# Kernel tuning notes

Measured on AMD Instinct MI355X. Metric: run time of the kernel, lower is better.

## Reference

```python
import jax, jax.numpy as jnp
import numpy as np
import math

D_MODEL = 1024
N_HEADS = 16
D_HEAD = D_MODEL // N_HEADS
D_FF = 4096
BATCH = 2
SEQ = 2048
EPS = 1e-5


def _rmsnorm(x, w):
    rms = jnp.sqrt(jnp.mean(x * x, axis=-1, keepdims=True) + EPS)
    return (x / rms) * w


def _gelu_erf(x):
    # matches 0.5 * x * (1 + erf(x / sqrt(2)))
    return 0.5 * x * (1.0 + jax.lax.erf(x / jnp.sqrt(jnp.asarray(2.0, x.dtype))))


def setup_inputs() -> dict:
    key = jax.random.key(0)
    ks = jax.random.split(key, 6)
    scale = 0.02
    x = jax.random.normal(ks[0], (BATCH, SEQ, D_MODEL), dtype=jnp.float32)
    w_qkv = jax.random.normal(ks[1], (3 * D_MODEL, D_MODEL), dtype=jnp.float32) * scale
    w_o = jax.random.normal(ks[2], (D_MODEL, D_MODEL), dtype=jnp.float32) * scale
    ln1_w = jnp.ones((D_MODEL,), dtype=jnp.float32)
    ln2_w = jnp.ones((D_MODEL,), dtype=jnp.float32)
    w1 = jax.random.normal(ks[3], (D_FF, D_MODEL), dtype=jnp.float32) * scale
    w2 = jax.random.normal(ks[4], (D_MODEL, D_FF), dtype=jnp.float32) * scale
    return {"x": x, "w_qkv": w_qkv, "w_o": w_o, "ln1_w": ln1_w,
            "ln2_w": ln2_w, "w1": w1, "w2": w2}


def reference(x, w_qkv, w_o, ln1_w, ln2_w, w1, w2):
    B, S, D = x.shape
    # --- attention sublayer (pre-norm) ---
    h = _rmsnorm(x, ln1_w)
    qkv = jnp.einsum('bsd,ed->bse', h, w_qkv)            # (B,S,3*D)
    qkv = qkv.reshape(B, S, 3, N_HEADS, D_HEAD)
    q, k, v = jnp.moveaxis(qkv, 2, 0)                    # each (B,S,H,dh)
    q = q.transpose(0, 2, 1, 3)                          # (B,H,S,dh)
    k = k.transpose(0, 2, 1, 3)
    v = v.transpose(0, 2, 1, 3)
    scores = jnp.einsum('bhqd,bhkd->bhqk', q, k) / math.sqrt(D_HEAD)
    causal = jnp.tril(jnp.ones((S, S), dtype=bool))      # True = keep
    scores = jnp.where(causal, scores, jnp.asarray(-jnp.inf, scores.dtype))
    attn = jax.nn.softmax(scores, axis=-1)
    ctx = jnp.einsum('bhqk,bhkd->bhqd', attn, v)         # (B,H,S,dh)
    ctx = ctx.transpose(0, 2, 1, 3).reshape(B, S, D)
    attn_out = jnp.einsum('bsd,ed->bse', ctx, w_o)
    first_sum = x + attn_out
    # --- FFN sublayer (pre-norm) ---
    h2 = _rmsnorm(first_sum, ln2_w)
    ff = jnp.einsum('bsf,df->bsd', _gelu_erf(jnp.einsum('bsd,fd->bsf', h2, w1)), w2)
    return first_sum + ff
```

## Files before the change

kernel.cpp:

```cpp
#include <hip/hip_runtime.h>

typedef unsigned short u16;
typedef unsigned int u32;
typedef __attribute__((ext_vector_type(8))) short short8;
typedef __attribute__((ext_vector_type(4))) float f32x4;

#define AS1 __attribute__((address_space(1)))
#define AS3 __attribute__((address_space(3)))

__device__ __forceinline__ u16 f2bf(float f) {
  union { float f; unsigned u; } v; v.f = f;
  return (u16)((v.u + 0x7fffu + ((v.u >> 16) & 1u)) >> 16);
}
__device__ __forceinline__ u32 pack2bf(float a, float b) {
  return (u32)f2bf(a) | ((u32)f2bf(b) << 16);
}
__device__ __forceinline__ u32 permpack(float a, float b) {
  union { float f; u32 u; } ua, ub; ua.f = a; ub.f = b;
  return __builtin_amdgcn_perm(ub.u, ua.u, 0x07060302u);
}

__global__ void cvt_kernel(const float* __restrict__ in, u16* __restrict__ out,
                           float scale) {
  int i = (blockIdx.x * 256 + threadIdx.x) * 4;
  float4 v = *(const float4*)(in + i);
  ushort4 o = make_ushort4(f2bf(v.x * scale), f2bf(v.y * scale),
                           f2bf(v.z * scale), f2bf(v.w * scale));
  *(ushort4*)(out + i) = o;
}

__global__ void rmsnorm_kernel(const float* __restrict__ x, const float* __restrict__ w,
                               u16* __restrict__ out) {
  const int row = blockIdx.x, tid = threadIdx.x;
  const float4 v = ((const float4*)(x + (size_t)row * 1024))[tid];
  float ss = v.x * v.x + v.y * v.y + v.z * v.z + v.w * v.w;
#pragma unroll
  for (int off = 32; off > 0; off >>= 1) ss += __shfl_xor(ss, off);
  __shared__ float red[4];
  if ((tid & 63) == 0) red[tid >> 6] = ss;
  __syncthreads();
  float tot = red[0] + red[1] + red[2] + red[3];
  float scale = 1.0f / sqrtf(tot * (1.0f / 1024.0f) + 1e-5f);
  const float4 wv = ((const float4*)w)[tid];
  ushort4 o = make_ushort4(f2bf(v.x * scale * wv.x), f2bf(v.y * scale * wv.y),
                           f2bf(v.z * scale * wv.z), f2bf(v.w * scale * wv.w));
  ((ushort4*)(out + (size_t)row * 1024))[tid] = o;
}

template <int EPI>
__global__ __launch_bounds__(256)
void gemm_bt(const u16* __restrict__ A, const u16* __restrict__ B,
             const float* __restrict__ RES, void* __restrict__ OUT,
             int M, int N, int K) {
  __shared__ __align__(16) u16 As[128 * 32];
  __shared__ __align__(16) u16 Bs[128 * 32];
  const int tid = threadIdx.x;
  const int wave = tid >> 6, lane = tid & 63;
  const int quad = lane >> 4, l16 = lane & 15;
  const int m0 = blockIdx.y * 128, n0 = blockIdx.x * 128;
  const int wm = (wave >> 1) * 64, wn = (wave & 1) * 64;
  f32x4 acc[4][4] = {};

  const int c0 = wave * 128 + lane;
  const int r0_row = c0 >> 2, r0_col = (c0 & 3) * 8;
  const int c1 = c0 + 64;
  const int r1_row = c1 >> 2, r1_col = (c1 & 3) * 8;

  for (int k0 = 0; k0 < K; k0 += 32) {
    __syncthreads();
    {
      u16* ga0 = (u16*)(A + (size_t)(m0 + r0_row) * K + k0 + r0_col);
      u16* ga1 = (u16*)(A + (size_t)(m0 + r1_row) * K + k0 + r1_col);
      u16* gb0 = (u16*)(B + (size_t)(n0 + r0_row) * K + k0 + r0_col);
      u16* gb1 = (u16*)(B + (size_t)(n0 + r1_row) * K + k0 + r1_col);
      __builtin_amdgcn_global_load_lds((AS1 void*)ga0, (AS3 void*)(As + wave * 1024), 16, 0, 0);
      __builtin_amdgcn_global_load_lds((AS1 void*)ga1, (AS3 void*)(As + wave * 1024 + 512), 16, 0, 0);
      __builtin_amdgcn_global_load_lds((AS1 void*)gb0, (AS3 void*)(Bs + wave * 1024), 16, 0, 0);
      __builtin_amdgcn_global_load_lds((AS1 void*)gb1, (AS3 void*)(Bs + wave * 1024 + 512), 16, 0, 0);
    }
    __syncthreads();
    short8 af[4], bfr[4];
#pragma unroll
    for (int i = 0; i < 4; ++i) {
      af[i]  = *(const short8*)(As + (wm + i * 16 + l16) * 32 + quad * 8);
      bfr[i] = *(const short8*)(Bs + (wn + i * 16 + l16) * 32 + quad * 8);
    }
#pragma unroll
    for (int i = 0; i < 4; ++i)
#pragma unroll
      for (int j = 0; j < 4; ++j)
        acc[i][j] = __builtin_amdgcn_mfma_f32_16x16x32_bf16(af[i], bfr[j], acc[i][j], 0, 0, 0);
  }

#pragma unroll
  for (int i = 0; i < 4; ++i) {
#pragma unroll
    for (int j = 0; j < 4; ++j) {
#pragma unroll
      for (int r = 0; r < 4; ++r) {
        int row = m0 + wm + i * 16 + quad * 4 + r;
        int col = n0 + wn + j * 16 + l16;
        size_t idx = (size_t)row * N + col;
        float v = acc[i][j][r];
        if constexpr (EPI == 0) {
          ((u16*)OUT)[idx] = f2bf(v);
        } else if constexpr (EPI == 1) {
          ((float*)OUT)[idx] = RES[idx] + v;
        } else {
          float g = 0.5f * v * (1.0f + erff(v * 0.70710678118654752f));
          ((u16*)OUT)[idx] = f2bf(g);
        }
      }
    }
  }
}

__global__ __launch_bounds__(256)
void packkv_kernel(const u16* __restrict__ qkv, u16* __restrict__ Kp,
                   u16* __restrict__ Vp) {
  __shared__ __align__(16) u16 Ks[32][72];
  __shared__ __align__(16) u16 Vs[32][72];
  const int kt = blockIdx.x, h = blockIdx.y, b = blockIdx.z;
  const int tid = threadIdx.x;
  const int key0 = kt * 32;
  {
    const size_t g = (size_t)b * 2048 * 3072 + (size_t)(key0 + (tid >> 3)) * 3072
                     + h * 64 + (tid & 7) * 8;
    *(short8*)(&Ks[tid >> 3][(tid & 7) * 8]) = *(const short8*)(qkv + g + 1024);
    *(short8*)(&Vs[tid >> 3][(tid & 7) * 8]) = *(const short8*)(qkv + g + 2048);
  }
  __syncthreads();
  const int wave = tid >> 6, lane = tid & 63;
  const int quad = lane >> 4, l16 = lane & 15;
  const int permrow = 8 * (l16 >> 2) + (l16 & 3);
  const size_t obase = ((size_t)((b * 16 + h) * 64 + kt)) * 2048 + tid * 8;
  {
    int row = permrow + (wave >> 1) * 4;
    int col = quad * 8 + (wave & 1) * 32;
    *(short8*)(Kp + obase) = *(const short8*)(&Ks[row][col]);
  }
  {
    short8 v;
    int col = wave * 16 + l16;
#pragma unroll
    for (int j = 0; j < 8; ++j) v[j] = (short)Vs[quad * 8 + j][col];
    *(short8*)(Vp + obase) = v;
  }
}

struct AttnState {
  f32x4 o0, o1, o2, o3;
  float ls;
};

template <bool MASKED>
__device__ __forceinline__ void attn_tile(
    AttnState& st, const u16* kp, const u16* vp, int key0, int q_abs, int quad,
    short8 qf0, short8 qf1) {
  short8 kf00 = *(const short8*)kp;
  short8 kf01 = *(const short8*)(kp + 512);
  short8 kf10 = *(const short8*)(kp + 1024);
  short8 kf11 = *(const short8*)(kp + 1536);
  short8 vf0 = *(const short8*)vp;
  short8 vf1 = *(const short8*)(vp + 512);
  short8 vf2 = *(const short8*)(vp + 1024);
  short8 vf3 = *(const short8*)(vp + 1536);

  f32x4 s0 = {}, s1 = {};
  s0 = __builtin_amdgcn_mfma_f32_16x16x32_bf16(kf00, qf0, s0, 0, 0, 0);
  s0 = __builtin_amdgcn_mfma_f32_16x16x32_bf16(kf01, qf1, s0, 0, 0, 0);
  s1 = __builtin_amdgcn_mfma_f32_16x16x32_bf16(kf10, qf0, s1, 0, 0, 0);
  s1 = __builtin_amdgcn_mfma_f32_16x16x32_bf16(kf11, qf1, s1, 0, 0, 0);

  float p[8];
#pragma unroll
  for (int r = 0; r < 4; ++r) {
    p[r]     = __expf(s0[r]);
    p[4 + r] = __expf(s1[r]);
  }
  if constexpr (MASKED) {
    const int kb = key0 + 8 * quad;
#pragma unroll
    for (int r = 0; r < 4; ++r) {
      if (kb + r > q_abs)     p[r] = 0.f;
      if (kb + 4 + r > q_abs) p[4 + r] = 0.f;
    }
  }
  st.ls += ((p[0] + p[1]) + (p[2] + p[3])) + ((p[4] + p[5]) + (p[6] + p[7]));

  union { u32 u[4]; short8 s; } pu;
  pu.u[0] = permpack(p[0], p[1]);
  pu.u[1] = permpack(p[2], p[3]);
  pu.u[2] = permpack(p[4], p[5]);
  pu.u[3] = permpack(p[6], p[7]);

  st.o0 = __builtin_amdgcn_mfma_f32_16x16x32_bf16(vf0, pu.s, st.o0, 0, 0, 0);
  st.o1 = __builtin_amdgcn_mfma_f32_16x16x32_bf16(vf1, pu.s, st.o1, 0, 0, 0);
  st.o2 = __builtin_amdgcn_mfma_f32_16x16x32_bf16(vf2, pu.s, st.o2, 0, 0, 0);
  st.o3 = __builtin_amdgcn_mfma_f32_16x16x32_bf16(vf3, pu.s, st.o3, 0, 0, 0);
}

__global__ __launch_bounds__(256)
void attn_kernel(const u16* __restrict__ qkv, const u16* __restrict__ Kpack,
                 const u16* __restrict__ Vpack, u16* __restrict__ ctx) {
  const int bx = blockIdx.x, by = blockIdx.y, bz = blockIdx.z;
  const int h = by, b = bz;
  const int qt = ((by >> 3) & 1) ? (31 - bx) : bx;
  const int tid = threadIdx.x, wave = tid >> 6, lane = tid & 63;
  const int quad = lane >> 4, l16 = lane & 15;
  const int q0 = qt * 64;
  const int qrow = q0 + wave * 16;
  const int q_abs = qrow + l16;
  const size_t base = (size_t)b * 2048 * 3072;
  const size_t headoff = (size_t)((b * 16 + h) * 64) * 2048;
  const u16* Kb = Kpack + headoff + lane * 8;
  const u16* Vb = Vpack + headoff + lane * 8;

  short8 qf0, qf1;
  {
    const u16* qp = qkv + base + (size_t)q_abs * 3072 + h * 64 + quad * 8;
    qf0 = *(const short8*)qp;
    qf1 = *(const short8*)(qp + 32);
  }
  AttnState st;
  st.o0 = f32x4{}; st.o1 = f32x4{}; st.o2 = f32x4{}; st.o3 = f32x4{};
  st.ls = 0.f;

  const int nfull = qrow >> 5;
  for (int kt = 0; kt < nfull; ++kt)
    attn_tile<false>(st, Kb + kt * 2048, Vb + kt * 2048, kt * 32, q_abs, quad, qf0, qf1);
  attn_tile<true>(st, Kb + nfull * 2048, Vb + nfull * 2048, nfull * 32, q_abs, quad, qf0, qf1);

  float ls = st.ls;
  ls += __shfl_xor(ls, 16);
  ls += __shfl_xor(ls, 32);
  float inv = 1.0f / ls;

  f32x4 o[4] = {st.o0, st.o1, st.o2, st.o3};
  u16* cp = ctx + (size_t)(b * 2048 + q_abs) * 1024 + h * 64 + quad * 4;
#pragma unroll
  for (int c = 0; c < 4; ++c) {
    u32 lo = pack2bf(o[c][0] * inv, o[c][1] * inv);
    u32 hi = pack2bf(o[c][2] * inv, o[c][3] * inv);
    *(uint2*)(cp + c * 16) = make_uint2(lo, hi);
  }
}

extern "C" void kernel_launch(void* const* d_in, const int* in_sizes, int n_in,
                              void* d_out, int out_size, void* d_ws, size_t ws_size,
                              hipStream_t stream) {
  const float* x     = (const float*)d_in[0];
  const float* w_qkv = (const float*)d_in[1];
  const float* w_o   = (const float*)d_in[2];
  const float* ln1   = (const float*)d_in[3];
  const float* ln2   = (const float*)d_in[4];
  const float* w1    = (const float*)d_in[5];
  const float* w2    = (const float*)d_in[6];
  float* out = (float*)d_out;

  char* p = (char*)d_ws;
  u16* wqkv_b = (u16*)p; p += (size_t)3072 * 1024 * 2;
  u16* wo_b   = (u16*)p; p += (size_t)1024 * 1024 * 2;
  u16* w1_b   = (u16*)p; p += (size_t)4096 * 1024 * 2;
  u16* w2_b   = (u16*)p; p += (size_t)1024 * 4096 * 2;
  u16* h_b    = (u16*)p; p += (size_t)4096 * 1024 * 2;
  u16* qkv_b  = (u16*)p;
  u16* g_b    = qkv_b;
  p += (size_t)4096 * 3072 * 2;
  u16* ctx_b  = (u16*)p; p += (size_t)4096 * 1024 * 2;
  float* fs   = (float*)p; p += (size_t)4096 * 1024 * 4;
  u16* kp_b   = (u16*)fs;
  u16* vp_b   = (u16*)fs + (size_t)4 * 1024 * 1024;

  cvt_kernel<<<1024, 256, 0, stream>>>(w_qkv, wqkv_b, 1.0f);
  cvt_kernel<<<1024, 256, 0, stream>>>(w_qkv + 1024 * 1024, wqkv_b + 1024 * 1024, 0.125f);
  cvt_kernel<<<1024, 256, 0, stream>>>(w_qkv + 2 * 1024 * 1024, wqkv_b + 2 * 1024 * 1024, 1.0f);
  cvt_kernel<<<1024, 256, 0, stream>>>(w_o, wo_b, 1.0f);
  cvt_kernel<<<4096, 256, 0, stream>>>(w1, w1_b, 1.0f);
  cvt_kernel<<<4096, 256, 0, stream>>>(w2, w2_b, 1.0f);

  rmsnorm_kernel<<<4096, 256, 0, stream>>>(x, ln1, h_b);
  gemm_bt<0><<<dim3(3072 / 128, 4096 / 128), 256, 0, stream>>>(h_b, wqkv_b, nullptr, qkv_b, 4096, 3072, 1024);
  packkv_kernel<<<dim3(64, 16, 2), 256, 0, stream>>>(qkv_b, kp_b, vp_b);
  attn_kernel<<<dim3(32, 16, 2), 256, 0, stream>>>(qkv_b, kp_b, vp_b, ctx_b);
  gemm_bt<1><<<dim3(1024 / 128, 4096 / 128), 256, 0, stream>>>(ctx_b, wo_b, x, fs, 4096, 1024, 1024);
  rmsnorm_kernel<<<4096, 256, 0, stream>>>(fs, ln2, h_b);
  gemm_bt<2><<<dim3(4096 / 128, 4096 / 128), 256, 0, stream>>>(h_b, w1_b, nullptr, g_b, 4096, 4096, 1024);
  gemm_bt<1><<<dim3(1024 / 128, 4096 / 128), 256, 0, stream>>>(g_b, w2_b, fs, out, 4096, 1024, 4096);
}
```

Baseline: 392.7 us.

## Add split-K for the FFN down-projection and XOR-swizzle GEMM LDS tiles

Adds a split-K mode to the GEMM. The final FFN down-projection (K=4096, 256 blocks) now launches 1024 blocks, each covering a quarter of K and writing fp32 partials. A separate reduce kernel then adds the residual and the four partials. The same change XOR-swizzles the column chunk of the LDS tiles to cut bank conflicts on the fragment reads. The cost is about 64MB of partial writes and reads plus an extra launch, and split-K only runs if the workspace is large enough.

Measured after the change: 390.5 us. About the same (-0.5%).

```diff
diff --git a/kernel.cpp b/kernel.cpp
--- a/kernel.cpp
+++ b/kernel.cpp
@@ -51,7 +51,7 @@
 __global__ __launch_bounds__(256)
 void gemm_bt(const u16* __restrict__ A, const u16* __restrict__ B,
              const float* __restrict__ RES, void* __restrict__ OUT,
-             int M, int N, int K) {
+             int M, int N, int K, int KS) {
   __shared__ __align__(16) u16 As[128 * 32];
   __shared__ __align__(16) u16 Bs[128 * 32];
   const int tid = threadIdx.x;
@@ -62,11 +62,12 @@
   f32x4 acc[4][4] = {};
 
   const int c0 = wave * 128 + lane;
-  const int r0_row = c0 >> 2, r0_col = (c0 & 3) * 8;
+  const int r0_row = c0 >> 2, r0_col = ((c0 & 3) ^ (r0_row & 3)) * 8;
   const int c1 = c0 + 64;
-  const int r1_row = c1 >> 2, r1_col = (c1 & 3) * 8;
-
-  for (int k0 = 0; k0 < K; k0 += 32) {
+  const int r1_row = c1 >> 2, r1_col = ((c1 & 3) ^ (r1_row & 3)) * 8;
+
+  const int kbeg = blockIdx.z * KS, kend = kbeg + KS;
+  for (int k0 = kbeg; k0 < kend; k0 += 32) {
     __syncthreads();
     {
       u16* ga0 = (u16*)(A + (size_t)(m0 + r0_row) * K + k0 + r0_col);
@@ -79,11 +80,12 @@
       __builtin_amdgcn_global_load_lds((AS1 void*)gb1, (AS3 void*)(Bs + wave * 1024 + 512), 16, 0, 0);
     }
     __syncthreads();
+    const int rcol = (quad ^ (l16 & 3)) * 8;
     short8 af[4], bfr[4];
 #pragma unroll
     for (int i = 0; i < 4; ++i) {
-      af[i]  = *(const short8*)(As + (wm + i * 16 + l16) * 32 + quad * 8);
-      bfr[i] = *(const short8*)(Bs + (wn + i * 16 + l16) * 32 + quad * 8);
+      af[i]  = *(const short8*)(As + (wm + i * 16 + l16) * 32 + rcol);
+      bfr[i] = *(const short8*)(Bs + (wn + i * 16 + l16) * 32 + rcol);
     }
 #pragma unroll
     for (int i = 0; i < 4; ++i)
@@ -92,6 +94,7 @@
         acc[i][j] = __builtin_amdgcn_mfma_f32_16x16x32_bf16(af[i], bfr[j], acc[i][j], 0, 0, 0);
   }
 
+  const size_t zoff = (size_t)blockIdx.z * M * N;
 #pragma unroll
   for (int i = 0; i < 4; ++i) {
 #pragma unroll
@@ -106,13 +109,31 @@
           ((u16*)OUT)[idx] = f2bf(v);
         } else if constexpr (EPI == 1) {
           ((float*)OUT)[idx] = RES[idx] + v;
-        } else {
+        } else if constexpr (EPI == 2) {
           float g = 0.5f * v * (1.0f + erff(v * 0.70710678118654752f));
           ((u16*)OUT)[idx] = f2bf(g);
+        } else {
+          ((float*)OUT)[zoff + idx] = v;
         }
       }
     }
   }
+}
+
+__global__ void reduce4_kernel(const float* __restrict__ fs,
+                               const float* __restrict__ P,
+                               float* __restrict__ out, size_t n) {
+  size_t i = ((size_t)blockIdx.x * 256 + threadIdx.x) * 4;
+  float4 a = *(const float4*)(fs + i);
+  float4 p0 = *(const float4*)(P + i);
+  float4 p1 = *(const float4*)(P + n + i);
+  float4 p2 = *(const float4*)(P + 2 * n + i);
+  float4 p3 = *(const float4*)(P + 3 * n + i);
+  float4 o = make_float4(a.x + ((p0.x + p1.x) + (p2.x + p3.x)),
+                         a.y + ((p0.y + p1.y) + (p2.y + p3.y)),
+                         a.z + ((p0.z + p1.z) + (p2.z + p3.z)),
+                         a.w + ((p0.w + p1.w) + (p2.w + p3.w)));
+  *(float4*)(out + i) = o;
 }
 
 __global__ __launch_bounds__(256)
@@ -271,6 +292,9 @@
   float* fs   = (float*)p; p += (size_t)4096 * 1024 * 4;
   u16* kp_b   = (u16*)fs;
   u16* vp_b   = (u16*)fs + (size_t)4 * 1024 * 1024;
+  float* Pbuf = (float*)p;
+  const size_t need = (size_t)(p - (char*)d_ws) + (size_t)4 * 4096 * 1024 * 4;
+  const bool splitk = ws_size >= need;
 
   cvt_kernel<<<1024, 256, 0, stream>>>(w_qkv, wqkv_b, 1.0f);
   cvt_kernel<<<1024, 256, 0, stream>>>(w_qkv + 1024 * 1024, wqkv_b + 1024 * 1024, 0.125f);
@@ -280,11 +304,16 @@
   cvt_kernel<<<4096, 256, 0, stream>>>(w2, w2_b, 1.0f);
 
   rmsnorm_kernel<<<4096, 256, 0, stream>>>(x, ln1, h_b);
-  gemm_bt<0><<<dim3(3072 / 128, 4096 / 128), 256, 0, stream>>>(h_b, wqkv_b, nullptr, qkv_b, 4096, 3072, 1024);
+  gemm_bt<0><<<dim3(24, 32, 1), 256, 0, stream>>>(h_b, wqkv_b, nullptr, qkv_b, 4096, 3072, 1024, 1024);
   packkv_kernel<<<dim3(64, 16, 2), 256, 0, stream>>>(qkv_b, kp_b, vp_b);
   attn_kernel<<<dim3(32, 16, 2), 256, 0, stream>>>(qkv_b, kp_b, vp_b, ctx_b);
-  gemm_bt<1><<<dim3(1024 / 128, 4096 / 128), 256, 0, stream>>>(ctx_b, wo_b, x, fs, 4096, 1024, 1024);
+  gemm_bt<1><<<dim3(8, 32, 1), 256, 0, stream>>>(ctx_b, wo_b, x, fs, 4096, 1024, 1024, 1024);
   rmsnorm_kernel<<<4096, 256, 0, stream>>>(fs, ln2, h_b);
-  gemm_bt<2><<<dim3(4096 / 128, 4096 / 128), 256, 0, stream>>>(h_b, w1_b, nullptr, g_b, 4096, 4096, 1024);
-  gemm_bt<1><<<dim3(1024 / 128, 4096 / 128), 256, 0, stream>>>(g_b, w2_b, fs, out, 4096, 1024, 4096);
-}
+  gemm_bt<2><<<dim3(32, 32, 1), 256, 0, stream>>>(h_b, w1_b, nullptr, g_b, 4096, 4096, 1024, 1024);
+  if (splitk) {
+    gemm_bt<3><<<dim3(8, 32, 4), 256, 0, stream>>>(g_b, w2_b, nullptr, Pbuf, 4096, 1024, 4096, 1024);
+    reduce4_kernel<<<4096, 256, 0, stream>>>(fs, Pbuf, out, (size_t)4096 * 1024);
+  } else {
+    gemm_bt<1><<<dim3(8, 32, 1), 256, 0, stream>>>(g_b, w2_b, fs, out, 4096, 1024, 4096, 4096);
+  }
+}
```
